# Kernel tuning notes

Hardware: AMD Instinct MI355X
Metric: run time of the kernel (lower is better)

## Reference

```python
import jax, jax.numpy as jnp
import numpy as np

KERNELS = ("gaussian", "laplacian", "gaussian", "laplacian")
N, M, D, N_PER = 384, 384, 64, 200


def setup_inputs():
    key = jax.random.key(0)
    kx, ky, kb, kp = jax.random.split(key, 4)
    X = jax.random.normal(kx, (N, D), dtype=jnp.float32)
    Y = jax.random.normal(ky, (M, D), dtype=jnp.float32)
    # positive bandwidths of realistic magnitude for d=64 gaussian/laplacian kernels
    bandwidths = jax.random.uniform(kb, (4,), dtype=jnp.float32) * 8.0 + 4.0
    # each row is a random permutation of n+m indices (torch.randperm equivalent)
    perms = jax.vmap(lambda k: jax.random.permutation(k, N + M))(
        jax.random.split(kp, N_PER)).astype(jnp.int32)
    return {"X": X, "Y": Y, "bandwidths": bandwidths, "perms": perms}


def _pairwise_dist(Z):
    # torch.cdist(Z, Z, p=2); eps keeps sqrt grad finite on the zero diagonal
    sq = jnp.sum(Z * Z, axis=1)
    d2 = jnp.maximum(sq[:, None] + sq[None, :] - 2.0 * (Z @ Z.T), 0.0)
    return jnp.sqrt(d2 + 1e-12)


def reference(X, Y, bandwidths, perms):
    n, m = X.shape[0], Y.shape[0]
    Z = jnp.concatenate([X, Y], axis=0)            # [n+m, d]
    dist = _pairwise_dist(Z)                        # [n+m, n+m]
    idx = jnp.arange(min(n, m))
    perm_X, perm_Y = perms[:, :n], perms[:, n:]    # [n_per, n], [n_per, m]
    U, U_b = [], []
    for i, kern in enumerate(KERNELS):
        b = bandwidths[i]
        if kern == "gaussian":
            K = jnp.exp(-(dist * dist) / (b * b))
        else:  # laplacian
            K = jnp.exp(-dist / b)
        # mmd_u's in-place K_XY[diag]=0 mutates the view of K, so zero first
        K = K.at[idx, n + idx].set(0.0)
        K_XX, K_YY, K_XY = K[:n, :n], K[n:, n:], K[:n, n:]
        mmd = ((K_XX.sum() - jnp.trace(K_XX)) / (n * (n - 1))
               + (K_YY.sum() - jnp.trace(K_YY)) / (m * (m - 1))
               - 2.0 * K_XY.sum() / (n * m))
        U.append(mmd)
        # fast_perm: gather permuted blocks, zero diagonals, reduce per permutation
        diagK = jnp.diagonal(K)
        sXX = K[perm_X[:, :, None], perm_X[:, None, :]].sum((1, 2)) - diagK[perm_X].sum(1)
        sYY = K[perm_Y[:, :, None], perm_Y[:, None, :]].sum((1, 2)) - diagK[perm_Y].sum(1)
        sXY = (K[perm_X[:, :, None], perm_Y[:, None, :]].sum((1, 2))
               - K[perm_X[:, idx], perm_Y[:, idx]].sum(1))
        U_b.append(sXX / (n * (n - 1)) + sYY / (m * (m - 1)) - 2.0 * sXY / (n * m))
    U = jnp.stack(U)[:, None]    # [n_b, 1]  == compute_U_stats U.unsqueeze(1)
    U_b = jnp.stack(U_b)         # [n_b, n_per]
    return jnp.concatenate([U, U_b], axis=1)  # [n_b, 1 + n_per]
```

## Files before the change

### kernel.cpp

```cpp
#include <hip/hip_runtime.h>
#include <hip/hip_cooperative_groups.h>

namespace cg = cooperative_groups;

#define NTOT 768
#define NHALF 384
#define DDIM 64
#define NPER 200
#define PPAD 256
#define NKER 4
#define NMB 12
#define NKH 2
#define NB_GEMM 384
#define NPART (NMB * NKH)
#define NTILE 12
#define LDSROW 68
#define NBLK_FUSED 400

typedef __attribute__((ext_vector_type(8))) short short8;
typedef __attribute__((ext_vector_type(4))) float floatx4;

constexpr int K0SZ  = NTOT * NTOT;
constexpr int OF_KH = 0;
constexpr int KH_FLOATS = NKER * K0SZ / 2;
constexpr int OF_P   = OF_KH + KH_FLOATS;
constexpr int OF_C   = OF_P + NKER * NTILE * NTOT;
constexpr int OF_ROWM = OF_C + NKER * NHALF;
constexpr int OF_COLM = OF_ROWM + NKER * NTOT;
constexpr int OF_SCAL = OF_COLM + NKER * NTOT;
constexpr int OF_STT  = OF_SCAL + 16;
constexpr int STT_FLOATS = PPAD * NTOT / 2;
constexpr int OF_Q0P  = OF_STT + STT_FLOATS;

__device__ __forceinline__ unsigned short f2bf(float f) {
    unsigned int u = __float_as_uint(f);
    return (unsigned short)((u + 0x7FFFu + ((u >> 16) & 1u)) >> 16);
}
__device__ __forceinline__ float bf2f(unsigned short h) {
    return __uint_as_float(((unsigned int)h) << 16);
}

__device__ __forceinline__ void phase1_body(int bid, int tid, float* smem,
                                            const float* __restrict__ X,
                                            const float* __restrict__ Y,
                                            const float* __restrict__ bw,
                                            const int* __restrict__ perms,
                                            float* __restrict__ ws) {
    float* zb  = smem;
    float* nrm = smem + 128 * LDSROW;
    unsigned short* STT = (unsigned short*)(ws + OF_STT);
    unsigned short* KH  = (unsigned short*)(ws + OF_KH);

    if (bid < NPER) {
        if (tid < 192) {
            ((uint2*)(STT + bid * NTOT))[tid] = make_uint2(0u, 0u);
            if (bid < PPAD - NPER)
                ((uint2*)(STT + (NPER + bid) * NTOT))[tid] = make_uint2(0u, 0u);
        }
        __syncthreads();
        int v = perms[bid * NTOT + tid];
        STT[bid * NTOT + v] = 0x3F80;
        if (tid < NHALF - 256) {
            int v2 = perms[bid * NTOT + 256 + tid];
            STT[bid * NTOT + v2] = 0x3F80;
        }
        return;
    }

    int t  = bid - NPER;
    int at = t / NTILE, bt = t % NTILE;
    int a0 = at * 64, b0 = bt * 64;
    int ta = tid >> 4, tb = tid & 15;

    float ib2[NKER], ib1[NKER];
#pragma unroll
    for (int k = 0; k < NKER; ++k) { float b = bw[k]; ib2[k] = 1.f / (b * b); ib1[k] = 1.f / b; }

#pragma unroll
    for (int it = 0; it < 8; ++it) {
        int idx = it * 256 + tid;
        int j = idx >> 4, qf = idx & 15;
        int g = (j < 64) ? a0 + j : b0 + (j - 64);
        const float* zr = (g < NHALF) ? X + g * DDIM : Y + (g - NHALF) * DDIM;
        *(float4*)(zb + j * LDSROW + qf * 4) = *(const float4*)(zr + qf * 4);
    }
    __syncthreads();
    if (tid < 128) {
        float s = 0.f;
        const float* zr = zb + tid * LDSROW;
#pragma unroll
        for (int d = 0; d < DDIM; d += 4) {
            float4 zv = *(const float4*)(zr + d);
            s += zv.x * zv.x + zv.y * zv.y + zv.z * zv.z + zv.w * zv.w;
        }
        nrm[tid] = s;
    }
    __syncthreads();

    float acc[4][4];
#pragma unroll
    for (int r = 0; r < 4; ++r)
#pragma unroll
        for (int c = 0; c < 4; ++c) acc[r][c] = 0.f;
#pragma unroll
    for (int s = 0; s < 16; ++s) {
        float4 av[4], bv[4];
#pragma unroll
        for (int r = 0; r < 4; ++r) av[r] = *(const float4*)(zb + (ta * 4 + r) * LDSROW + s * 4);
#pragma unroll
        for (int c = 0; c < 4; ++c) bv[c] = *(const float4*)(zb + (64 + tb * 4 + c) * LDSROW + s * 4);
#pragma unroll
        for (int r = 0; r < 4; ++r)
#pragma unroll
            for (int c = 0; c < 4; ++c) {
                acc[r][c] = fmaf(av[r].x, bv[c].x, acc[r][c]);
                acc[r][c] = fmaf(av[r].y, bv[c].y, acc[r][c]);
                acc[r][c] = fmaf(av[r].z, bv[c].z, acc[r][c]);
                acc[r][c] = fmaf(av[r].w, bv[c].w, acc[r][c]);
            }
    }

    float rs[4][NKER];
#pragma unroll
    for (int r = 0; r < 4; ++r)
#pragma unroll
        for (int k = 0; k < NKER; ++k) rs[r][k] = 0.f;

#pragma unroll
    for (int r = 0; r < 4; ++r) {
        int a = a0 + ta * 4 + r;
        ushort4 us[NKER];
#pragma unroll
        for (int c = 0; c < 4; ++c) {
            int b = b0 + tb * 4 + c;
            float d2 = (nrm[ta * 4 + r] + nrm[64 + tb * 4 + c]) - 2.f * acc[r][c];
            if (b == a) d2 = 0.f;
            d2 = fmaxf(d2, 0.f);
            float d2e = d2 + 1e-12f;
            float dist = sqrtf(d2e);
#pragma unroll
            for (int k = 0; k < NKER; ++k) {
                float val = ((k & 1) == 0) ? __expf(-d2e * ib2[k]) : __expf(-dist * ib1[k]);
                rs[r][k] += val;
                unsigned short h = f2bf(val);
                if (c == 0) us[k].x = h; else if (c == 1) us[k].y = h;
                else if (c == 2) us[k].z = h; else us[k].w = h;
                if (bt == at + 6 && tb == ta && c == r)
                    ws[OF_C + k * NHALF + a] = val;
            }
        }
#pragma unroll
        for (int k = 0; k < NKER; ++k)
            *(ushort4*)(KH + k * K0SZ + a * NTOT + b0 + tb * 4) = us[k];
    }

#pragma unroll
    for (int off = 8; off > 0; off >>= 1)
#pragma unroll
        for (int r = 0; r < 4; ++r)
#pragma unroll
            for (int k = 0; k < NKER; ++k) rs[r][k] += __shfl_down(rs[r][k], off, 64);
    if (tb == 0) {
#pragma unroll
        for (int k = 0; k < NKER; ++k) {
            float4 pv = make_float4(rs[0][k], rs[1][k], rs[2][k], rs[3][k]);
            *(float4*)(ws + OF_P + (k * NTILE + bt) * NTOT + a0 + ta * 4) = pv;
        }
    }
}

__device__ __forceinline__ void phase2_body(int bid, int tid, float* smem,
                                            const float* __restrict__ bw,
                                            float* __restrict__ ws,
                                            float* __restrict__ out) {
    int wave = tid >> 6, lane = tid & 63;

    if (bid < NB_GEMM) {
        int mb = bid % NMB;
        int t  = bid / NMB;
        int nc = t & 3;
        int t2 = t >> 2;
        int k  = t2 & 3;
        int kh = t2 >> 2;
        int m0 = mb * 64 + wave * 16;
        int n0 = nc * 64;
        int row = lane & 15, quad = lane >> 4;
        const unsigned short* KH  = (const unsigned short*)(ws + OF_KH);
        const unsigned short* STT = (const unsigned short*)(ws + OF_STT);
        const unsigned short* aptr = KH + k * K0SZ + (m0 + row) * NTOT + quad * 8;
        floatx4 acc[4][2];
#pragma unroll
        for (int j = 0; j < 4; ++j)
#pragma unroll
            for (int h = 0; h < 2; ++h) acc[j][h] = (floatx4){0.f, 0.f, 0.f, 0.f};
        int kk0 = kh * (NTOT / 2);
        for (int kk = kk0; kk < kk0 + NTOT / 2; kk += 64) {
            short8 a0 = *(const short8*)(aptr + kk);
            short8 a1 = *(const short8*)(aptr + kk + 32);
#pragma unroll
            for (int j = 0; j < 4; ++j) {
                const unsigned short* bp = STT + (n0 + j * 16 + row) * NTOT + quad * 8 + kk;
                short8 b0 = *(const short8*)(bp);
                short8 b1 = *(const short8*)(bp + 32);
                acc[j][0] = __builtin_amdgcn_mfma_f32_16x16x32_bf16(a0, b0, acc[j][0], 0, 0, 0);
                acc[j][1] = __builtin_amdgcn_mfma_f32_16x16x32_bf16(a1, b1, acc[j][1], 0, 0, 0);
            }
        }
        __syncthreads();
#pragma unroll
        for (int j = 0; j < 4; ++j) {
            const unsigned short* sp = STT + (n0 + j * 16 + row) * NTOT + m0 + quad * 4;
            float p = 0.f;
#pragma unroll
            for (int r = 0; r < 4; ++r) p += (acc[j][0][r] + acc[j][1][r]) * bf2f(sp[r]);
            p += __shfl_down(p, 32, 64);
            p += __shfl_down(p, 16, 64);
            if (lane < 16) smem[wave * 64 + j * 16 + lane] = p;
        }
        __syncthreads();
        if (tid < 64) {
            float s = smem[tid] + smem[64 + tid] + smem[128 + tid] + smem[192 + tid];
            ws[OF_Q0P + (k * NPART + kh * NMB + mb) * PPAD + n0 + tid] = s;
        }
        return;
    }

    int k = bid - NB_GEMM;
    const float* Pk = ws + OF_P + k * (NTILE * NTOT);
    float v[5] = {0.f, 0.f, 0.f, 0.f, 0.f};
    for (int a = tid; a < NTOT; a += 256) {
        float rsx = 0.f, rsy = 0.f;
#pragma unroll
        for (int j = 0; j < 6; ++j)  rsx += Pk[j * NTOT + a];
#pragma unroll
        for (int j = 6; j < 12; ++j) rsy += Pk[j * NTOT + a];
        float rs0 = rsx + rsy;
        float cx = (a < NHALF)  ? ws[OF_C + k * NHALF + a] : 0.f;
        float cy = (a >= NHALF) ? ws[OF_C + k * NHALF + a - NHALF] : 0.f;
        ws[OF_ROWM + k * NTOT + a] = rs0 - cx;
        ws[OF_COLM + k * NTOT + a] = rs0 - cy;
        v[0] += rs0;
        if (a < NHALF) { v[1] += cx; v[2] += rsx; v[4] += rsy; }
        else           { v[3] += rsy; }
    }
#pragma unroll
    for (int off = 32; off > 0; off >>= 1)
#pragma unroll
        for (int j = 0; j < 5; ++j) v[j] += __shfl_down(v[j], off, 64);
    __syncthreads();
    if (lane == 0)
#pragma unroll
        for (int j = 0; j < 5; ++j) smem[wave * 8 + j] = v[j];
    __syncthreads();
    if (tid == 0) {
        float tot0 = smem[0] + smem[8] + smem[16] + smem[24];
        float csum = smem[1] + smem[9] + smem[17] + smem[25];
        float sxx  = smem[2] + smem[10] + smem[18] + smem[26];
        float syy  = smem[3] + smem[11] + smem[19] + smem[27];
        float sxy  = smem[4] + smem[12] + smem[20] + smem[28];
        float b = bw[k];
        float dist0 = sqrtf(1e-12f);
        float dk = ((k & 1) == 0) ? expf(-(dist0 * dist0) / (b * b)) : expf(-dist0 / b);
        ws[OF_SCAL + k * 4 + 0] = tot0 - csum;
        ws[OF_SCAL + k * 4 + 1] = dk;
        double U = ((double)sxx - 384.0 * (double)dk) * (1.0 / 147072.0)
                 + ((double)syy - 384.0 * (double)dk) * (1.0 / 147072.0)
                 - 2.0 * ((double)sxy - (double)csum) * (1.0 / 147456.0);
        out[k * 201] = (float)U;
    }
}

__device__ __forceinline__ void phase3_body(int bid, int tid, float* smem,
                                            const int* __restrict__ perms,
                                            const float* __restrict__ ws,
                                            float* __restrict__ out) {
    int wave = tid >> 6, lane = tid & 63;
    int p  = bid % NPER;
    int kb = bid / NPER;
    int k0 = kb, k1 = kb + 2;
    const unsigned short* STT = (const unsigned short*)(ws + OF_STT);
    const unsigned short* KH  = (const unsigned short*)(ws + OF_KH);
    float v0[4] = {0.f, 0.f, 0.f, 0.f};
    float v1[4] = {0.f, 0.f, 0.f, 0.f};
    for (int i = tid; i < NHALF; i += 256) {
        int a  = perms[p * NTOT + i];
        int bY = perms[p * NTOT + NHALF + i];
        float ss = bf2f(STT[p * NTOT + i]) * bf2f(STT[p * NTOT + NHALF + i]);
        bool diag = (a < NHALF) && (bY == a + NHALF);
        v0[0] += ws[OF_ROWM + k0 * NTOT + a];
        v0[1] += ws[OF_COLM + k0 * NTOT + a];
        float kv0 = bf2f(KH[k0 * K0SZ + a * NTOT + bY]);
        v0[2] += diag ? 0.f : kv0;
        v0[3] += ws[OF_C + k0 * NHALF + i] * ss;
        v1[0] += ws[OF_ROWM + k1 * NTOT + a];
        v1[1] += ws[OF_COLM + k1 * NTOT + a];
        float kv1 = bf2f(KH[k1 * K0SZ + a * NTOT + bY]);
        v1[2] += diag ? 0.f : kv1;
        v1[3] += ws[OF_C + k1 * NHALF + i] * ss;
    }
#pragma unroll
    for (int off = 32; off > 0; off >>= 1)
#pragma unroll
        for (int j = 0; j < 4; ++j) {
            v0[j] += __shfl_down(v0[j], off, 64);
            v1[j] += __shfl_down(v1[j], off, 64);
        }
    if (lane == 0)
#pragma unroll
        for (int j = 0; j < 4; ++j) {
            smem[wave * 8 + j]     = v0[j];
            smem[wave * 8 + 4 + j] = v1[j];
        }
    float q0 = 0.f, q1 = 0.f;
    if (tid < NPART) {
        q0 = ws[OF_Q0P + (k0 * NPART + tid) * PPAD + p];
        q1 = ws[OF_Q0P + (k1 * NPART + tid) * PPAD + p];
    }
#pragma unroll
    for (int off = 16; off > 0; off >>= 1) {
        q0 += __shfl_down(q0, off, 32);
        q1 += __shfl_down(q1, off, 32);
    }
    __syncthreads();
    if (tid == 0) {
#pragma unroll
        for (int kk = 0; kk < 2; ++kk) {
            int k = (kk == 0) ? k0 : k1;
            int o = (kk == 0) ? 0 : 4;
            float qsumf = (kk == 0) ? q0 : q1;
            double rs   = (double)(smem[o + 0] + smem[o + 8] + smem[o + 16] + smem[o + 24]);
            double cs   = (double)(smem[o + 1] + smem[o + 9] + smem[o + 17] + smem[o + 25]);
            double pair = (double)(smem[o + 2] + smem[o + 10] + smem[o + 18] + smem[o + 26]);
            double qc   = (double)(smem[o + 3] + smem[o + 11] + smem[o + 19] + smem[o + 27]);
            double total_mod = (double)ws[OF_SCAL + k * 4 + 0];
            double dk        = (double)ws[OF_SCAL + k * 4 + 1];
            double q = (double)qsumf - qc;
            double sXX = q - 384.0 * dk;
            double sYY = total_mod - rs - cs + q - 384.0 * dk;
            double sXY = rs - q - pair;
            out[k * 201 + 1 + p] =
                (float)(sXX * (1.0 / 147072.0) + sYY * (1.0 / 147072.0) - 2.0 * sXY * (1.0 / 147456.0));
        }
    }
}

__global__ __launch_bounds__(256, 2) void k_fused(const float* __restrict__ X,
                                                  const float* __restrict__ Y,
                                                  const float* __restrict__ bw,
                                                  const int* __restrict__ perms,
                                                  float* __restrict__ ws,
                                                  float* __restrict__ out) {
    __shared__ float smem[128 * LDSROW + 128];
    cg::grid_group grid = cg::this_grid();
    int bid = blockIdx.x, tid = threadIdx.x;

    if (bid < NPER + NTILE * NTILE) phase1_body(bid, tid, smem, X, Y, bw, perms, ws);
    __threadfence();
    grid.sync();

    if (bid < NB_GEMM + NKER) phase2_body(bid, tid, smem, bw, ws, out);
    __threadfence();
    grid.sync();

    phase3_body(bid, tid, smem, perms, ws, out);
}

__global__ __launch_bounds__(256) void k_s1(const float* __restrict__ X,
                                            const float* __restrict__ Y,
                                            const float* __restrict__ bw,
                                            const int* __restrict__ perms,
                                            float* __restrict__ ws) {
    __shared__ float smem[128 * LDSROW + 128];
    phase1_body(blockIdx.x, threadIdx.x, smem, X, Y, bw, perms, ws);
}

__global__ __launch_bounds__(256) void k_s2(const float* __restrict__ bw,
                                            float* __restrict__ ws, float* __restrict__ out) {
    __shared__ float smem[256];
    phase2_body(blockIdx.x, threadIdx.x, smem, bw, ws, out);
}

__global__ __launch_bounds__(256) void k_s3(const int* __restrict__ perms,
                                            const float* __restrict__ ws,
                                            float* __restrict__ out) {
    __shared__ float smem[64];
    phase3_body(blockIdx.x, threadIdx.x, smem, perms, ws, out);
}

extern "C" void kernel_launch(void* const* d_in, const int* in_sizes, int n_in,
                              void* d_out, int out_size, void* d_ws, size_t ws_size,
                              hipStream_t stream) {
    const float* X     = (const float*)d_in[0];
    const float* Y     = (const float*)d_in[1];
    const float* bw    = (const float*)d_in[2];
    const int*   perms = (const int*)d_in[3];
    float* ws  = (float*)d_ws;
    float* out = (float*)d_out;

    static int coop_ok = -1;
    if (coop_ok < 0) {
        int nb = 0;
        hipError_t e = hipOccupancyMaxActiveBlocksPerMultiprocessor(&nb, k_fused, 256, 0);
        coop_ok = (e == hipSuccess && nb >= 2) ? 1 : 0;
    }
    if (coop_ok == 1) {
        void* args[6] = {(void*)&X, (void*)&Y, (void*)&bw, (void*)&perms, (void*)&ws, (void*)&out};
        if (hipLaunchCooperativeKernel(k_fused, dim3(NBLK_FUSED), dim3(256), args, 0u, stream)
            == hipSuccess)
            return;
        coop_ok = 0;
    }
    k_s1<<<NPER + NTILE * NTILE, 256, 0, stream>>>(X, Y, bw, perms, ws);
    k_s2<<<NB_GEMM + NKER, 256, 0, stream>>>(bw, ws, out);
    k_s3<<<NBLK_FUSED, 256, 0, stream>>>(perms, ws, out);
}
```

Baseline: 102.8 us.

## Interleave four kernels' values per element so phase 3 gathers all kernels at once

Phase 1 now also writes an interleaved bf16 copy of the kernel matrix with all four kernels adjacent per (a,b) pair, and the per-row/column margins and diagonal terms are stored kernel-interleaved. Phase 3 uses one block per permutation that handles all four kernels with single vector gathers instead of two blocks each doing two kernels, and the grid shrinks to 388 blocks. This cuts the number of scattered random gathers in phase 3 and the redundant perm/STT loads. In exchange phase 1 writes an extra full copy of the kernel matrix, adding global write traffic.

```diff
diff --git a/kernel.cpp b/kernel.cpp
--- a/kernel.cpp
+++ b/kernel.cpp
@@ -15,7 +15,7 @@
 #define NPART (NMB * NKH)
 #define NTILE 12
 #define LDSROW 68
-#define NBLK_FUSED 400
+#define NBLK_FUSED 388
 
 typedef __attribute__((ext_vector_type(8))) short short8;
 typedef __attribute__((ext_vector_type(4))) float floatx4;
@@ -31,6 +31,7 @@
 constexpr int OF_STT  = OF_SCAL + 16;
 constexpr int STT_FLOATS = PPAD * NTOT / 2;
 constexpr int OF_Q0P  = OF_STT + STT_FLOATS;
+constexpr int OF_KH2  = OF_Q0P + NKER * NPART * PPAD;
 
 __device__ __forceinline__ unsigned short f2bf(float f) {
     unsigned int u = __float_as_uint(f);
@@ -50,6 +51,7 @@
     float* nrm = smem + 128 * LDSROW;
     unsigned short* STT = (unsigned short*)(ws + OF_STT);
     unsigned short* KH  = (unsigned short*)(ws + OF_KH);
+    unsigned short* KH2 = (unsigned short*)(ws + OF_KH2);
 
     if (bid < NPER) {
         if (tid < 192) {
@@ -129,7 +131,7 @@
 #pragma unroll
     for (int r = 0; r < 4; ++r) {
         int a = a0 + ta * 4 + r;
-        ushort4 us[NKER];
+        unsigned short h[4][4];
 #pragma unroll
         for (int c = 0; c < 4; ++c) {
             int b = b0 + tb * 4 + c;
@@ -142,16 +144,30 @@
             for (int k = 0; k < NKER; ++k) {
                 float val = ((k & 1) == 0) ? __expf(-d2e * ib2[k]) : __expf(-dist * ib1[k]);
                 rs[r][k] += val;
-                unsigned short h = f2bf(val);
-                if (c == 0) us[k].x = h; else if (c == 1) us[k].y = h;
-                else if (c == 2) us[k].z = h; else us[k].w = h;
+                h[c][k] = f2bf(val);
                 if (bt == at + 6 && tb == ta && c == r)
-                    ws[OF_C + k * NHALF + a] = val;
+                    ws[OF_C + a * 4 + k] = val;
             }
         }
 #pragma unroll
-        for (int k = 0; k < NKER; ++k)
-            *(ushort4*)(KH + k * K0SZ + a * NTOT + b0 + tb * 4) = us[k];
+        for (int k = 0; k < NKER; ++k) {
+            ushort4 us;
+            us.x = h[0][k]; us.y = h[1][k]; us.z = h[2][k]; us.w = h[3][k];
+            *(ushort4*)(KH + k * K0SZ + a * NTOT + b0 + tb * 4) = us;
+        }
+        {
+            unsigned short* p2 = KH2 + (a * NTOT + b0 + tb * 4) * 4;
+            short8 lo, hi;
+#pragma unroll
+            for (int k = 0; k < NKER; ++k) {
+                lo[k]     = (short)h[0][k];
+                lo[4 + k] = (short)h[1][k];
+                hi[k]     = (short)h[2][k];
+                hi[4 + k] = (short)h[3][k];
+            }
+            *(short8*)(p2)     = lo;
+            *(short8*)(p2 + 8) = hi;
+        }
     }
 
 #pragma unroll
@@ -235,10 +251,10 @@
 #pragma unroll
         for (int j = 6; j < 12; ++j) rsy += Pk[j * NTOT + a];
         float rs0 = rsx + rsy;
-        float cx = (a < NHALF)  ? ws[OF_C + k * NHALF + a] : 0.f;
-        float cy = (a >= NHALF) ? ws[OF_C + k * NHALF + a - NHALF] : 0.f;
-        ws[OF_ROWM + k * NTOT + a] = rs0 - cx;
-        ws[OF_COLM + k * NTOT + a] = rs0 - cy;
+        float cx = (a < NHALF)  ? ws[OF_C + a * 4 + k] : 0.f;
+        float cy = (a >= NHALF) ? ws[OF_C + (a - NHALF) * 4 + k] : 0.f;
+        ws[OF_ROWM + a * 4 + k] = rs0 - cx;
+        ws[OF_COLM + a * 4 + k] = rs0 - cy;
         v[0] += rs0;
         if (a < NHALF) { v[1] += cx; v[2] += rsx; v[4] += rsy; }
         else           { v[3] += rsy; }
@@ -274,73 +290,76 @@
                                             const int* __restrict__ perms,
                                             const float* __restrict__ ws,
                                             float* __restrict__ out) {
+    if (bid >= NPER) return;
     int wave = tid >> 6, lane = tid & 63;
-    int p  = bid % NPER;
-    int kb = bid / NPER;
-    int k0 = kb, k1 = kb + 2;
+    int p = bid;
     const unsigned short* STT = (const unsigned short*)(ws + OF_STT);
-    const unsigned short* KH  = (const unsigned short*)(ws + OF_KH);
-    float v0[4] = {0.f, 0.f, 0.f, 0.f};
-    float v1[4] = {0.f, 0.f, 0.f, 0.f};
+    const unsigned short* KH2 = (const unsigned short*)(ws + OF_KH2);
+    float v[NKER][4];
+#pragma unroll
+    for (int k = 0; k < NKER; ++k)
+#pragma unroll
+        for (int j = 0; j < 4; ++j) v[k][j] = 0.f;
+
     for (int i = tid; i < NHALF; i += 256) {
         int a  = perms[p * NTOT + i];
         int bY = perms[p * NTOT + NHALF + i];
         float ss = bf2f(STT[p * NTOT + i]) * bf2f(STT[p * NTOT + NHALF + i]);
         bool diag = (a < NHALF) && (bY == a + NHALF);
-        v0[0] += ws[OF_ROWM + k0 * NTOT + a];
-        v0[1] += ws[OF_COLM + k0 * NTOT + a];
-        float kv0 = bf2f(KH[k0 * K0SZ + a * NTOT + bY]);
-        v0[2] += diag ? 0.f : kv0;
-        v0[3] += ws[OF_C + k0 * NHALF + i] * ss;
-        v1[0] += ws[OF_ROWM + k1 * NTOT + a];
-        v1[1] += ws[OF_COLM + k1 * NTOT + a];
-        float kv1 = bf2f(KH[k1 * K0SZ + a * NTOT + bY]);
-        v1[2] += diag ? 0.f : kv1;
-        v1[3] += ws[OF_C + k1 * NHALF + i] * ss;
+        float4 rw = *(const float4*)(ws + OF_ROWM + a * 4);
+        float4 cl = *(const float4*)(ws + OF_COLM + a * 4);
+        float4 cc = *(const float4*)(ws + OF_C + i * 4);
+        ushort4 kv = *(const ushort4*)(KH2 + (a * NTOT + bY) * 4);
+        float rwk[4] = {rw.x, rw.y, rw.z, rw.w};
+        float clk[4] = {cl.x, cl.y, cl.z, cl.w};
+        float cck[4] = {cc.x, cc.y, cc.z, cc.w};
+        float kvk[4] = {bf2f(kv.x), bf2f(kv.y), bf2f(kv.z), bf2f(kv.w)};
+#pragma unroll
+        for (int k = 0; k < NKER; ++k) {
+            v[k][0] += rwk[k];
+            v[k][1] += clk[k];
+            v[k][2] += diag ? 0.f : kvk[k];
+            v[k][3] += cck[k] * ss;
+        }
     }
 #pragma unroll
     for (int off = 32; off > 0; off >>= 1)
 #pragma unroll
-        for (int j = 0; j < 4; ++j) {
-            v0[j] += __shfl_down(v0[j], off, 64);
-            v1[j] += __shfl_down(v1[j], off, 64);
-        }
+        for (int k = 0; k < NKER; ++k)
+#pragma unroll
+            for (int j = 0; j < 4; ++j) v[k][j] += __shfl_down(v[k][j], off, 64);
     if (lane == 0)
 #pragma unroll
-        for (int j = 0; j < 4; ++j) {
-            smem[wave * 8 + j]     = v0[j];
-            smem[wave * 8 + 4 + j] = v1[j];
-        }
-    float q0 = 0.f, q1 = 0.f;
-    if (tid < NPART) {
-        q0 = ws[OF_Q0P + (k0 * NPART + tid) * PPAD + p];
-        q1 = ws[OF_Q0P + (k1 * NPART + tid) * PPAD + p];
-    }
-#pragma unroll
-    for (int off = 16; off > 0; off >>= 1) {
-        q0 += __shfl_down(q0, off, 32);
-        q1 += __shfl_down(q1, off, 32);
-    }
+        for (int k = 0; k < NKER; ++k)
+#pragma unroll
+            for (int j = 0; j < 4; ++j) smem[wave * 16 + k * 4 + j] = v[k][j];
+
+    float q = 0.f;
+    if (lane < NPART) q = ws[OF_Q0P + (wave * NPART + lane) * PPAD + p];
+#pragma unroll
+    for (int off = 16; off > 0; off >>= 1) q += __shfl_down(q, off, 32);
+    if (lane == 0) smem[64 + wave] = q;
     __syncthreads();
-    if (tid == 0) {
-#pragma unroll
-        for (int kk = 0; kk < 2; ++kk) {
-            int k = (kk == 0) ? k0 : k1;
-            int o = (kk == 0) ? 0 : 4;
-            float qsumf = (kk == 0) ? q0 : q1;
-            double rs   = (double)(smem[o + 0] + smem[o + 8] + smem[o + 16] + smem[o + 24]);
-            double cs   = (double)(smem[o + 1] + smem[o + 9] + smem[o + 17] + smem[o + 25]);
-            double pair = (double)(smem[o + 2] + smem[o + 10] + smem[o + 18] + smem[o + 26]);
-            double qc   = (double)(smem[o + 3] + smem[o + 11] + smem[o + 19] + smem[o + 27]);
-            double total_mod = (double)ws[OF_SCAL + k * 4 + 0];
-            double dk        = (double)ws[OF_SCAL + k * 4 + 1];
-            double q = (double)qsumf - qc;
-            double sXX = q - 384.0 * dk;
-            double sYY = total_mod - rs - cs + q - 384.0 * dk;
-            double sXY = rs - q - pair;
-            out[k * 201 + 1 + p] =
-                (float)(sXX * (1.0 / 147072.0) + sYY * (1.0 / 147072.0) - 2.0 * sXY * (1.0 / 147456.0));
-        }
+
+    if (tid < NKER) {
+        int k = tid;
+        float rsf = 0.f, csf = 0.f, pairf = 0.f, qcf = 0.f;
+#pragma unroll
+        for (int w = 0; w < 4; ++w) {
+            rsf   += smem[w * 16 + k * 4 + 0];
+            csf   += smem[w * 16 + k * 4 + 1];
+            pairf += smem[w * 16 + k * 4 + 2];
+            qcf   += smem[w * 16 + k * 4 + 3];
+        }
+        double rs = (double)rsf, cs = (double)csf, pair = (double)pairf, qc = (double)qcf;
+        double total_mod = (double)ws[OF_SCAL + k * 4 + 0];
+        double dk        = (double)ws[OF_SCAL + k * 4 + 1];
+        double qd = (double)smem[64 + k] - qc;
+        double sXX = qd - 384.0 * dk;
+        double sYY = total_mod - rs - cs + qd - 384.0 * dk;
+        double sXY = rs - qd - pair;
+        out[k * 201 + 1 + p] =
+            (float)(sXX * (1.0 / 147072.0) + sYY * (1.0 / 147072.0) - 2.0 * sXY * (1.0 / 147456.0));
     }
 }
 
@@ -383,7 +402,7 @@
 __global__ __launch_bounds__(256) void k_s3(const int* __restrict__ perms,
                                             const float* __restrict__ ws,
                                             float* __restrict__ out) {
-    __shared__ float smem[64];
+    __shared__ float smem[128];
     phase3_body(blockIdx.x, threadIdx.x, smem, perms, ws, out);
 }
 
@@ -412,5 +431,5 @@
     }
     k_s1<<<NPER + NTILE * NTILE, 256, 0, stream>>>(X, Y, bw, perms, ws);
     k_s2<<<NB_GEMM + NKER, 256, 0, stream>>>(bw, ws, out);
-    k_s3<<<NBLK_FUSED, 256, 0, stream>>>(perms, ws, out);
-}
+    k_s3<<<NPER, 256, 0, stream>>>(perms, ws, out);
+}
```

Measured after the change: 104.6 us. About the same (+1.8%).
